# Optimization experiments

Measured on AMD Instinct MI355X. Metric: run time of the kernel, lower is better.

The kernel has to match this reference:

```python
import jax, jax.numpy as jnp
import numpy as np

B, IN, U = 16, 1024, 1024


def _wSw(W, S):
    # W: [i,u], S: [b,i,i] -> W^T S W : [b,u,u]
    return jnp.einsum('iu,bij,jv->buv', W, S, W)


def _xSx(x, Wsig):
    # (sum_i x_i^2) * W_Sigma, broadcast over batch
    return jnp.sum(x * x, axis=1)[:, None, None] * Wsig


def _trS(S, Wsig):
    return jnp.trace(S, axis1=1, axis2=2)[:, None, None] * Wsig


def _hadamard_sigma(s1, s2, m1, m2):
    # s1*s2 + diag(m1) s2 diag(m1) + diag(m2) s1 diag(m2)
    return (s1 * s2
            + m1[:, :, None] * s2 * m1[:, None, :]
            + m2[:, :, None] * s1 * m2[:, None, :])


def _act_sigma(g, S):
    # S * outer(g, g)
    return S * (g[:, :, None] * g[:, None, :])


def setup_inputs() -> dict:
    key = jax.random.key(0)
    ks = jax.random.split(key, 16)
    f32 = jnp.float32
    init_mu, ini_sigma = 0.05, -4.6
    inp = {
        'mu_inputs': jax.random.normal(ks[0], (B, IN), f32),
        'sigma_inputs': 0.01 * jax.random.normal(ks[1], (B, IN, IN), f32),
        'prev_state': 0.1 * jax.random.normal(ks[2], (B, U), f32),
        'Sigma_state': 0.01 * jax.random.normal(ks[3], (B, U, U), f32),
        'U_z': init_mu * jax.random.normal(ks[4], (IN, U), f32),
        'uz_sigma': jnp.full((U,), ini_sigma, f32),
        'W_z': init_mu * jax.random.normal(ks[5], (U, U), f32),
        'wz_sigma': jnp.full((U,), ini_sigma, f32),
        'U_r': init_mu * jax.random.normal(ks[6], (IN, U), f32),
        'ur_sigma': jnp.full((U,), ini_sigma, f32),
        'W_r': init_mu * jax.random.normal(ks[7], (U, U), f32),
        'wr_sigma': jnp.full((U,), ini_sigma, f32),
        'U_h': init_mu * jax.random.normal(ks[8], (IN, U), f32),
        'uh_sigma': jnp.full((U,), ini_sigma, f32),
        'W_h': init_mu * jax.random.normal(ks[9], (U, U), f32),
        'wh_sigma': jnp.full((U,), ini_sigma, f32),
    }
    return inp


def reference(mu_inputs, sigma_inputs, prev_state, Sigma_state,
              U_z, uz_sigma, W_z, wz_sigma,
              U_r, ur_sigma, W_r, wr_sigma,
              U_h, uh_sigma, W_h, wh_sigma):
    sp = jax.nn.softplus
    # ---- z gate ----
    pre_z = mu_inputs @ U_z + prev_state @ W_z
    z = jax.nn.sigmoid(pre_z)
    Uz_S, Wz_S = jnp.diag(sp(uz_sigma)), jnp.diag(sp(wz_sigma))
    Sigma_zz = (_wSw(U_z, sigma_inputs) + _xSx(mu_inputs, Uz_S) + _trS(sigma_inputs, Uz_S)
                + _wSw(W_z, Sigma_state) + _xSx(prev_state, Wz_S) + _trS(Sigma_state, Wz_S))
    Sigma_z = _act_sigma(z * (1.0 - z), Sigma_zz)  # analytic d sigmoid
    # ---- r gate ----
    pre_r = mu_inputs @ U_r + prev_state @ W_r
    r = jax.nn.sigmoid(pre_r)
    Ur_S, Wr_S = jnp.diag(sp(ur_sigma)), jnp.diag(sp(wr_sigma))
    Sigma_rr = (_wSw(U_r, sigma_inputs) + _xSx(mu_inputs, Ur_S) + _trS(sigma_inputs, Ur_S)
                + _wSw(W_r, Sigma_state) + _xSx(prev_state, Wr_S) + _trS(Sigma_state, Wr_S))
    Sigma_r = _act_sigma(r * (1.0 - r), Sigma_rr)
    # ---- h gate ----
    sr = prev_state * r
    pre_h = mu_inputs @ U_h + sr @ W_h
    h = jnp.tanh(pre_h)
    Uh_S, Wh_S = jnp.diag(sp(uh_sigma)), jnp.diag(sp(wh_sigma))
    sigma_g = _hadamard_sigma(Sigma_state, Sigma_r, prev_state, r)
    Sigma_hh = (_wSw(U_h, sigma_inputs) + _xSx(mu_inputs, Uh_S) + _trS(sigma_inputs, Uh_S)
                + _wSw(W_h, sigma_g) + _xSx(sr, Wh_S) + _trS(sigma_g, Wh_S))
    Sigma_h = _act_sigma(1.0 - h * h, Sigma_hh)  # analytic d tanh
    # ---- combine ----
    mu_out = z * prev_state + (1.0 - z) * h
    sigma_a = _hadamard_sigma(Sigma_z, Sigma_state, z, prev_state)
    sigma_b = _hadamard_sigma(Sigma_z, Sigma_h, 1.0 - z, h)
    sigma_ab = Sigma_z * (prev_state[:, :, None] * h[:, None, :])
    sigma_abT = Sigma_z * (h[:, :, None] * prev_state[:, None, :])
    Sigma_out = sigma_a + sigma_b - sigma_ab - sigma_abT
    Sigma_out = jnp.where(jnp.isfinite(Sigma_out), Sigma_out, jnp.zeros_like(Sigma_out))
    eye = jnp.eye(Sigma_out.shape[-1], dtype=bool)
    Sigma_out = jnp.where(eye, jnp.abs(Sigma_out), Sigma_out)
    return mu_out, Sigma_out
```

## Files before the change

kernel.cpp:

```cpp
#include <hip/hip_runtime.h>
#include <math.h>


#define B_  16
#define N_  1024
#define NN_ (1024*1024)

typedef __bf16 bf16x8 __attribute__((ext_vector_type(8)));
typedef float  f32x4  __attribute__((ext_vector_type(4)));
typedef unsigned short ushort8v __attribute__((ext_vector_type(8)));

__device__ __forceinline__ unsigned short f2bf(float f) {
  union { float f; unsigned int u; } v; v.f = f;
  unsigned int r = v.u + 0x7fffu + ((v.u >> 16) & 1u);
  return (unsigned short)(r >> 16);
}
__device__ __forceinline__ float bf2f(unsigned short h) {
  union { unsigned int u; float f; } v; v.u = ((unsigned int)h) << 16;
  return v.f;
}
__device__ __forceinline__ float f4get(const float4& v, int q) {
  return q == 0 ? v.x : (q == 1 ? v.y : (q == 2 ? v.z : v.w));
}
__device__ __forceinline__ unsigned short u4get(const ushort4& v, int q) {
  return q == 0 ? v.x : (q == 1 ? v.y : (q == 2 ? v.z : v.w));
}

__device__ __forceinline__ void gload_lds16(const void* g, void* l) {
  __builtin_amdgcn_global_load_lds((__attribute__((address_space(1))) void*)g,
                                   (__attribute__((address_space(3))) void*)l,
                                   16, 0, 0);
}

#define MFMA_ __builtin_amdgcn_mfma_f32_16x16x32_bf16

template<int OMODE, int PAIR>
__global__ __launch_bounds__(512)
void gemm8p(const unsigned short* __restrict__ A, int lda, long aStride, int koffA,
            const unsigned short* __restrict__ Bm, const unsigned short* __restrict__ Bm2,
            int ldb, long bStride, int K,
            void* __restrict__ Out, int ldo, long oStride, int noff,
            const float* __restrict__ act,
            const float* __restrict__ spU, const float* __restrict__ spW,
            const float* __restrict__ dU, const float* __restrict__ dW)
{
  __shared__ __align__(16) char ldsb[131072];
  const int id = blockIdx.x;
  const int xcd = id & 7, rest = id >> 3;
  const int mt = rest & 3, pp = rest >> 2;
  const int panel = xcd + (pp << 3);
  const int nt = panel & 3;
  const int b  = (panel >> 2) & 15;
  const int ps = PAIR ? (panel >> 6) : 0;
  const unsigned short* Bsel = (PAIR && ps) ? Bm2 : Bm;
  const int kofx = koffA + (ps ? 1024 : 0);
  const int nofx = noff  + (ps ? 1024 : 0);
  const int mbase = mt << 8, nbase = nt << 8;
  const int tid = threadIdx.x, lane = tid & 63, w = tid >> 6;
  const int wm = w >> 2, wn = w & 3;
  const int NT = K >> 6;

  f32x4 acc[8][4];
  const f32x4 zero4 = {0.f, 0.f, 0.f, 0.f};
#pragma unroll
  for (int i = 0; i < 8; i++)
#pragma unroll
    for (int j = 0; j < 4; j++) acc[i][j] = zero4;

  const int l3 = lane >> 3, l7 = lane & 7;
  const int posg = l7 ^ l3;
  const int gr = (l3 << 1) + (posg >> 2);
  const int gc = (posg & 3) << 3;
  const int bi0 = w << 1, bi1 = bi0 + 1;
  const int rS0 = ((bi0 >> 1) << 4) + gr, cS0 = ((bi0 & 1) << 5) + gc;
  const int rS1 = ((bi1 >> 1) << 4) + gr, cS1 = ((bi1 & 1) << 5) + gc;
  const unsigned short* Ab = A + (size_t)b * aStride + (size_t)mbase * lda + kofx;
  const unsigned short* Bb = Bsel + (size_t)b * bStride + (size_t)nbase * ldb;
  const int d0 = w << 11, d1 = (w << 11) + 1024;

  auto SA = [&](int tt, int h) {
    char* dst = ldsb + ((tt & 1) << 16) + (h << 14);
    const unsigned short* s = Ab + (size_t)(h << 7) * lda + ((size_t)tt << 6);
    gload_lds16(s + (size_t)rS0 * lda + cS0, dst + d0);
    gload_lds16(s + (size_t)rS1 * lda + cS1, dst + d1);
  };
  auto SB = [&](int tt, int h) {
    char* dst = ldsb + ((tt & 1) << 16) + 32768 + (h << 14);
    const unsigned short* s = Bb + (size_t)(h << 7) * ldb + ((size_t)tt << 6);
    gload_lds16(s + (size_t)rS0 * ldb + cS0, dst + d0);
    gload_lds16(s + (size_t)rS1 * ldb + cS1, dst + d1);
  };

  const int lrow = lane & 15, c4 = lane >> 4;
  const int aoff = ((lrow >> 1) << 7) + (((((lrow & 1) << 2) | c4) ^ (lrow >> 1)) << 4);
  const int abase = wm << 14;
  const int bbase = 32768 + ((wn >> 1) << 14);
  const int brg   = (wn & 1) << 2;
  auto LDA = [&](const char* pb, int mi, int ks) -> bf16x8 {
    return *(const bf16x8*)(pb + abase + (((mi << 1) + ks) << 10) + aoff);
  };
  auto LDB = [&](const char* pb, int ni, int ks) -> bf16x8 {
    return *(const bf16x8*)(pb + bbase + ((((brg + ni) << 1) + ks) << 10) + aoff);
  };

  SA(0, 0); SA(0, 1); SB(0, 0); SB(0, 1);
  if (NT > 1) { SB(1, 0); SB(1, 1); }
  asm volatile("s_waitcnt vmcnt(4)" ::: "memory");
  __builtin_amdgcn_sched_barrier(0);
  __builtin_amdgcn_s_barrier();
  __builtin_amdgcn_sched_barrier(0);

  bf16x8 av[4], bv[4];
  for (int kt = 0; kt < NT; ++kt) {
    const char* pb = ldsb + ((kt & 1) << 16);
#pragma unroll
    for (int mi = 0; mi < 4; mi++) av[mi] = LDA(pb, mi, 0);
#pragma unroll
    for (int ni = 0; ni < 4; ni++) bv[ni] = LDB(pb, ni, 0);
    if (kt + 1 < NT) SA(kt + 1, 0);
    __builtin_amdgcn_s_barrier();
    asm volatile("s_waitcnt lgkmcnt(0)" ::: "memory");
    __builtin_amdgcn_sched_barrier(0);
    __builtin_amdgcn_s_setprio(1);
#pragma unroll
    for (int ni = 0; ni < 4; ni++)
#pragma unroll
      for (int mi = 0; mi < 4; mi++)
        acc[mi][ni] = MFMA_(av[mi], bv[ni], acc[mi][ni], 0, 0, 0);
    __builtin_amdgcn_s_setprio(0);
    __builtin_amdgcn_sched_barrier(0);
    __builtin_amdgcn_s_barrier();
#pragma unroll
    for (int mi = 0; mi < 4; mi++) av[mi] = LDA(pb, 4 + mi, 0);
    if (kt + 1 < NT) SA(kt + 1, 1);
    __builtin_amdgcn_s_barrier();
    asm volatile("s_waitcnt lgkmcnt(0)" ::: "memory");
    __builtin_amdgcn_sched_barrier(0);
    __builtin_amdgcn_s_setprio(1);
#pragma unroll
    for (int ni = 0; ni < 4; ni++)
#pragma unroll
      for (int mi = 0; mi < 4; mi++)
        acc[4 + mi][ni] = MFMA_(av[mi], bv[ni], acc[4 + mi][ni], 0, 0, 0);
    __builtin_amdgcn_s_setprio(0);
    __builtin_amdgcn_sched_barrier(0);
    __builtin_amdgcn_s_barrier();
#pragma unroll
    for (int mi = 0; mi < 4; mi++) av[mi] = LDA(pb, mi, 1);
#pragma unroll
    for (int ni = 0; ni < 4; ni++) bv[ni] = LDB(pb, ni, 1);
    __builtin_amdgcn_s_barrier();
    asm volatile("s_waitcnt lgkmcnt(0)" ::: "memory");
    __builtin_amdgcn_sched_barrier(0);
    __builtin_amdgcn_s_setprio(1);
#pragma unroll
    for (int ni = 0; ni < 4; ni++)
#pragma unroll
      for (int mi = 0; mi < 4; mi++)
        acc[mi][ni] = MFMA_(av[mi], bv[ni], acc[mi][ni], 0, 0, 0);
    __builtin_amdgcn_s_setprio(0);
    __builtin_amdgcn_sched_barrier(0);
    __builtin_amdgcn_s_barrier();
#pragma unroll
    for (int mi = 0; mi < 4; mi++) av[mi] = LDA(pb, 4 + mi, 1);
    if (kt + 2 < NT) {
      SB(kt + 2, 0); SB(kt + 2, 1);
      asm volatile("s_waitcnt vmcnt(4)" ::: "memory");
    } else {
      asm volatile("s_waitcnt vmcnt(0)" ::: "memory");
    }
    __builtin_amdgcn_s_barrier();
    asm volatile("s_waitcnt lgkmcnt(0)" ::: "memory");
    __builtin_amdgcn_sched_barrier(0);
    __builtin_amdgcn_s_setprio(1);
#pragma unroll
    for (int ni = 0; ni < 4; ni++)
#pragma unroll
      for (int mi = 0; mi < 4; mi++)
        acc[4 + mi][ni] = MFMA_(av[mi], bv[ni], acc[4 + mi][ni], 0, 0, 0);
    __builtin_amdgcn_s_setprio(0);
    __builtin_amdgcn_sched_barrier(0);
    __builtin_amdgcn_s_barrier();
  }

  if (OMODE == 2) {
    const float* actb = act + b * N_;
    const float dUb = dU[b], dWb = dW[b];
#pragma unroll
    for (int mi = 0; mi < 8; mi++) {
      const int u0 = mbase + wm * 128 + mi * 16 + ((lane >> 4) << 2);
#pragma unroll
      for (int ni = 0; ni < 4; ni++) {
        const int v = nbase + wn * 64 + ni * 16 + (lane & 15);
        const float avv = actb[v];
#pragma unroll
        for (int r = 0; r < 4; r++) {
          const int u = u0 + r;
          float val = acc[mi][ni][r];
          if (u == v) val += dUb * spU[u] + dWb * spW[u];
          val *= actb[u] * avv;
          ((float*)Out)[(size_t)b * oStride + (size_t)u * ldo + v] = val;
        }
      }
    }
  } else {
    __syncthreads();
    unsigned short* scr = (unsigned short*)(ldsb + w * 16384);
    const float* actb = (OMODE == 1) ? (act + b * N_) : nullptr;
    float dUb = 0.f, dWb = 0.f;
    if (OMODE == 1) { dUb = dU[b]; dWb = dW[b]; }
#pragma unroll
    for (int mi = 0; mi < 8; mi++) {
      const int rl0 = mi * 16 + ((lane >> 4) << 2);
#pragma unroll
      for (int ni = 0; ni < 4; ni++) {
        const int cl = ni * 16 + (lane & 15);
#pragma unroll
        for (int r = 0; r < 4; r++) {
          const int rl = rl0 + r;
          float val = acc[mi][ni][r];
          if (OMODE == 1) {
            const int u = mbase + wm * 128 + rl, v = nbase + wn * 64 + cl;
            if (u == v) val += dUb * spU[u] + dWb * spW[u];
            val *= actb[u] * actb[v];
          }
          scr[rl * 64 + ((((cl >> 3) ^ (rl & 7))) << 3) + (cl & 7)] = f2bf(val);
        }
      }
    }
    asm volatile("s_waitcnt lgkmcnt(0)" ::: "memory");
    __builtin_amdgcn_sched_barrier(0);
    unsigned short* ob = (unsigned short*)Out + (size_t)b * oStride
        + (size_t)(mbase + wm * 128) * ldo + nofx + nbase + wn * 64;
#pragma unroll
    for (int pq = 0; pq < 16; pq++) {
      const int row = pq * 8 + (lane >> 3);
      const int ch = (lane & 7) ^ (row & 7);
      ushort8v vv = *(const ushort8v*)&scr[row * 64 + ((lane & 7) << 3)];
      *(ushort8v*)(ob + (size_t)row * ldo + ch * 8) = vv;
    }
  }
}


__global__ void conv_bf16(const float* __restrict__ in, unsigned short* __restrict__ out, int n4)
{
  int i = blockIdx.x * 256 + threadIdx.x;
  const int stride = gridDim.x * 256;
  for (; i < n4; i += stride) {
    const float4 v = ((const float4*)in)[i];
    ushort4 o;
    o.x = f2bf(v.x); o.y = f2bf(v.y); o.z = f2bf(v.z); o.w = f2bf(v.w);
    ((ushort4*)out)[i] = o;
  }
}

__global__ void build_AT(const float* __restrict__ Uz, const float* __restrict__ Wz,
                         const float* __restrict__ Ur, const float* __restrict__ Wr,
                         const float* __restrict__ Uh, const float* __restrict__ Wh,
                         unsigned short* __restrict__ AT)
{
  __shared__ float tile[32][33];
  const int g = blockIdx.z;
  const float* U = g == 0 ? Uz : (g == 1 ? Ur : Uh);
  const float* W = g == 0 ? Wz : (g == 1 ? Wr : Wh);
  const int u0  = blockIdx.x * 32;
  const int k0g = blockIdx.y * 32;
  const float* src = (k0g >= 1024) ? W : U;
  const int kloc = k0g & 1023;
  const int tx = threadIdx.x & 31, ty = threadIdx.x >> 5;
  unsigned short* out = AT + (size_t)g * N_ * 2048;
#pragma unroll
  for (int i = 0; i < 32; i += 8) tile[ty + i][tx] = src[(size_t)(kloc + ty + i) * N_ + u0 + tx];
  __syncthreads();
#pragma unroll
  for (int i = 0; i < 32; i += 8)
    out[(size_t)(u0 + ty + i) * 2048 + k0g + tx] = f2bf(tile[tx][ty + i]);
}

__global__ void softplus6(const float* a0, const float* a1, const float* a2,
                          const float* a3, const float* a4, const float* a5,
                          float* __restrict__ sp)
{
  const float* src[6] = {a0, a1, a2, a3, a4, a5};
  const int g = blockIdx.x;
  const float* s = src[g];
  for (int i = threadIdx.x; i < N_; i += 256) {
    float x = s[i];
    sp[g * N_ + i] = (x > 20.f) ? x : log1pf(expf(x));
  }
}

__global__ void scalars1(const float* __restrict__ mu, const float* __restrict__ prev,
                         const float* __restrict__ sin_, const float* __restrict__ Sst,
                         float* __restrict__ dA, float* __restrict__ dBzr)
{
  __shared__ float red[256];
  const int b = blockIdx.x;
  float s1 = 0.f, s2 = 0.f;
  for (int i = threadIdx.x; i < N_; i += 256) {
    const float m = mu[b * N_ + i];
    s1 += m * m + sin_[(size_t)b * NN_ + (size_t)i * (N_ + 1)];
    const float p = prev[b * N_ + i];
    s2 += p * p + Sst[(size_t)b * NN_ + (size_t)i * (N_ + 1)];
  }
  red[threadIdx.x] = s1; __syncthreads();
  for (int s = 128; s > 0; s >>= 1) { if (threadIdx.x < s) red[threadIdx.x] += red[threadIdx.x + s]; __syncthreads(); }
  if (threadIdx.x == 0) dA[b] = red[0];
  __syncthreads();
  red[threadIdx.x] = s2; __syncthreads();
  for (int s = 128; s > 0; s >>= 1) { if (threadIdx.x < s) red[threadIdx.x] += red[threadIdx.x + s]; __syncthreads(); }
  if (threadIdx.x == 0) dBzr[b] = red[0];
}

__global__ __launch_bounds__(256)
void gate_pre2(const float* __restrict__ x1, const float* __restrict__ x2,
               const float* __restrict__ U0, const float* __restrict__ W0,
               const float* __restrict__ U1, const float* __restrict__ W1,
               float* __restrict__ Ppart)
{
  const int g  = blockIdx.z;
  const int ks = blockIdx.y;
  const int out = blockIdx.x * 256 + threadIdx.x;
  const int b = out >> 10, col = out & 1023;
  const float* x = (ks < 4) ? x1 : x2;
  const float* Wm = (g == 0) ? ((ks < 4) ? U0 : W0) : ((ks < 4) ? U1 : W1);
  const int k0 = (ks & 3) * 256;
  const float* xb = x + b * N_ + k0;
  const float* wp = Wm + (size_t)k0 * N_ + col;
  float acc = 0.f;
#pragma unroll 8
  for (int k = 0; k < 256; k++)
    acc += xb[k] * wp[(size_t)k * N_];
  Ppart[(g * 8 + ks) * (B_ * N_) + out] = acc;
}

__global__ void gate_act2(const float* __restrict__ P,
                          float* __restrict__ z, float* __restrict__ gz,
                          float* __restrict__ r, float* __restrict__ gr)
{
  const int out = blockIdx.x * 256 + threadIdx.x;
  float a0 = 0.f, a1 = 0.f;
#pragma unroll
  for (int ks = 0; ks < 8; ks++) {
    a0 += P[ks * (B_ * N_) + out];
    a1 += P[(8 + ks) * (B_ * N_) + out];
  }
  const float s0 = 1.f / (1.f + expf(-a0));
  const float s1 = 1.f / (1.f + expf(-a1));
  z[out] = s0; gz[out] = s0 * (1.f - s0);
  r[out] = s1; gr[out] = s1 * (1.f - s1);
}

__global__ __launch_bounds__(256)
void gate_pre1(const float* __restrict__ x1, const float* __restrict__ x2,
               const float* __restrict__ U0, const float* __restrict__ W0,
               float* __restrict__ Ppart)
{
  const int ks = blockIdx.y;
  const int out = blockIdx.x * 256 + threadIdx.x;
  const int b = out >> 10, col = out & 1023;
  const float* x = (ks < 4) ? x1 : x2;
  const float* Wm = (ks < 4) ? U0 : W0;
  const int k0 = (ks & 3) * 256;
  const float* xb = x + b * N_ + k0;
  const float* wp = Wm + (size_t)k0 * N_ + col;
  float acc = 0.f;
#pragma unroll 8
  for (int k = 0; k < 256; k++)
    acc += xb[k] * wp[(size_t)k * N_];
  Ppart[ks * (B_ * N_) + out] = acc;
}

__global__ void gate_act1(const float* __restrict__ P,
                          float* __restrict__ h, float* __restrict__ gh)
{
  const int out = blockIdx.x * 256 + threadIdx.x;
  float a0 = 0.f;
#pragma unroll
  for (int ks = 0; ks < 8; ks++) a0 += P[ks * (B_ * N_) + out];
  const float s = tanhf(a0);
  h[out] = s; gh[out] = 1.f - s * s;
}

__global__ void sr_csr(const float* __restrict__ prev, const float* __restrict__ r,
                       float* __restrict__ sr, float* __restrict__ csr)
{
  __shared__ float red[256];
  const int b = blockIdx.x;
  float s = 0.f;
  for (int i = threadIdx.x; i < N_; i += 256) {
    const float v = prev[b * N_ + i] * r[b * N_ + i];
    sr[b * N_ + i] = v;
    s += v * v;
  }
  red[threadIdx.x] = s; __syncthreads();
  for (int k = 128; k > 0; k >>= 1) { if (threadIdx.x < k) red[threadIdx.x] += red[threadIdx.x + k]; __syncthreads(); }
  if (threadIdx.x == 0) csr[b] = red[0];
}

__global__ void hadamard_sg(const float* __restrict__ Sst, unsigned short* __restrict__ Sg,
                            const float* __restrict__ prev, const float* __restrict__ r)
{
  const size_t idx = ((size_t)blockIdx.x * 256 + threadIdx.x) * 4;
  const int b = (int)(idx >> 20);
  const int rem = (int)(idx & (NN_ - 1));
  const int i = rem >> 10, j0 = rem & 1023;
  const float pi = prev[b * N_ + i], ri = r[b * N_ + i];
  const float4  ss  = *(const float4*)(Sst + (size_t)b * NN_ + rem);
  const ushort4 sr4 = *(const ushort4*)(Sg + (size_t)b * NN_ + rem);
  ushort4 o;
  unsigned short* op = (unsigned short*)&o;
#pragma unroll
  for (int q = 0; q < 4; q++) {
    const float srv = bf2f(u4get(sr4, q));
    const float stv = f4get(ss, q);
    const float pj = prev[b * N_ + j0 + q];
    const float rj = r[b * N_ + j0 + q];
    op[q] = f2bf(stv * srv + pi * pj * srv + ri * rj * stv);
  }
  *(ushort4*)(Sg + (size_t)b * NN_ + rem) = o;
}

__global__ void scalars2(const unsigned short* __restrict__ Sg,
                         const float* __restrict__ csr, float* __restrict__ dBh)
{
  __shared__ float red[256];
  const int b = blockIdx.x;
  float s = 0.f;
  for (int i = threadIdx.x; i < N_; i += 256)
    s += bf2f(Sg[(size_t)b * NN_ + (size_t)i * (N_ + 1)]);
  red[threadIdx.x] = s; __syncthreads();
  for (int k = 128; k > 0; k >>= 1) { if (threadIdx.x < k) red[threadIdx.x] += red[threadIdx.x + k]; __syncthreads(); }
  if (threadIdx.x == 0) dBh[b] = red[0] + csr[b];
}

__global__ void mu_kernel(const float* __restrict__ z, const float* __restrict__ prev,
                          const float* __restrict__ h, float* __restrict__ mu_out)
{
  const int i = blockIdx.x * 256 + threadIdx.x;
  const float zz = z[i];
  mu_out[i] = zz * prev[i] + (1.f - zz) * h[i];
}

__global__ void combine(const unsigned short* __restrict__ Sz, const float* __restrict__ Sst,
                        const float* __restrict__ z, const float* __restrict__ prev,
                        const float* __restrict__ h, float* __restrict__ SigOut)
{
  const int row = blockIdx.x;
  const int b = row >> 10, u = row & 1023;
  const float zu = z[b * N_ + u], pu = prev[b * N_ + u], hu = h[b * N_ + u];
  const size_t base = (size_t)b * NN_ + (size_t)u * N_;
  const int j0 = threadIdx.x * 4;
  const ushort4 s4 = *(const ushort4*)(Sz + base + j0);
  const float4 sh = *(const float4*)(SigOut + base + j0);
  const float4 st = *(const float4*)(Sst + base + j0);
  const float4 zv = *(const float4*)(z + b * N_ + j0);
  const float4 pv = *(const float4*)(prev + b * N_ + j0);
  const float4 hv = *(const float4*)(h + b * N_ + j0);
  float o[4];
#pragma unroll
  for (int q = 0; q < 4; q++) {
    const int v = j0 + q;
    const float sz  = bf2f(u4get(s4, q));
    const float shh = f4get(sh, q);
    const float stt = f4get(st, q);
    const float zvv = f4get(zv, q);
    const float pvv = f4get(pv, q);
    const float hvv = f4get(hv, q);
    float res = sz * stt + zu * zvv * stt + pu * pvv * sz
              + sz * shh + (1.f - zu) * (1.f - zvv) * shh + hu * hvv * sz
              - sz * (pu * hvv) - sz * (hu * pvv);
    if (!isfinite(res)) res = 0.f;
    if (u == v) res = fabsf(res);
    o[q] = res;
  }
  float4 ov; ov.x = o[0]; ov.y = o[1]; ov.z = o[2]; ov.w = o[3];
  *(float4*)(SigOut + base + j0) = ov;
}


extern "C" void kernel_launch(void* const* d_in, const int* in_sizes, int n_in,
                              void* d_out, int out_size, void* d_ws, size_t ws_size,
                              hipStream_t stream)
{
  const float* mu   = (const float*)d_in[0];
  const float* sin_ = (const float*)d_in[1];
  const float* prev = (const float*)d_in[2];
  const float* Sst  = (const float*)d_in[3];
  const float* Uz = (const float*)d_in[4];  const float* uzs = (const float*)d_in[5];
  const float* Wz = (const float*)d_in[6];  const float* wzs = (const float*)d_in[7];
  const float* Ur = (const float*)d_in[8];  const float* urs = (const float*)d_in[9];
  const float* Wr = (const float*)d_in[10]; const float* wrs = (const float*)d_in[11];
  const float* Uh = (const float*)d_in[12]; const float* uhs = (const float*)d_in[13];
  const float* Wh = (const float*)d_in[14]; const float* whs = (const float*)d_in[15];

  char* ws = (char*)d_ws;
  size_t off = 0;
  auto take = [&](size_t bytes) -> char* {
    char* p = ws + off;
    off = (off + bytes + 255) & ~(size_t)255;
    return p;
  };
  unsigned short* Tcm = (unsigned short*)take((size_t)B_ * 2048 * 1024 * 2);
  unsigned short* Sz  = (unsigned short*)take((size_t)B_ * NN_ * 2);
  unsigned short* Sg  = (unsigned short*)take((size_t)B_ * NN_ * 2);
  unsigned short* AT  = (unsigned short*)take((size_t)3 * N_ * 2048 * 2);
  float* Ppart = (float*)take((size_t)16 * B_ * N_ * 4);
  float* sp   = (float*)take(6 * N_ * 4);
  float* z    = (float*)take(B_ * N_ * 4);
  float* gz   = (float*)take(B_ * N_ * 4);
  float* rr   = (float*)take(B_ * N_ * 4);
  float* gr   = (float*)take(B_ * N_ * 4);
  float* h    = (float*)take(B_ * N_ * 4);
  float* gh   = (float*)take(B_ * N_ * 4);
  float* sr   = (float*)take(B_ * N_ * 4);
  float* dA   = (float*)take(64);
  float* dBzr = (float*)take(64);
  float* dBh  = (float*)take(64);
  float* csr  = (float*)take(64);
  if (off > ws_size) return;

  float* mu_out = (float*)d_out;
  float* SigOut = (float*)d_out + (size_t)B_ * N_;
  unsigned short* SinH = (unsigned short*)SigOut;
  unsigned short* SstH = (unsigned short*)SigOut + (size_t)B_ * NN_;

  const unsigned short* ATz = AT;
  const unsigned short* ATr = AT + (size_t)N_ * 2048;
  const unsigned short* ATh = AT + (size_t)2 * N_ * 2048;

  conv_bf16<<<2048, 256, 0, stream>>>(sin_, SinH, B_ * NN_ / 4);
  conv_bf16<<<2048, 256, 0, stream>>>(Sst,  SstH, B_ * NN_ / 4);
  softplus6<<<6, 256, 0, stream>>>(uzs, wzs, urs, wrs, uhs, whs, sp);
  scalars1<<<16, 256, 0, stream>>>(mu, prev, sin_, Sst, dA, dBzr);
  build_AT<<<dim3(32, 64, 3), 256, 0, stream>>>(Uz, Wz, Ur, Wr, Uh, Wh, AT);
  gate_pre2<<<dim3(64, 8, 2), 256, 0, stream>>>(mu, prev, Uz, Wz, Ur, Wr, Ppart);
  gate_act2<<<64, 256, 0, stream>>>(Ppart, z, gz, rr, gr);
  sr_csr<<<16, 256, 0, stream>>>(prev, rr, sr, csr);
  gate_pre1<<<dim3(64, 8), 256, 0, stream>>>(mu, sr, Uh, Wh, Ppart);
  gate_act1<<<64, 256, 0, stream>>>(Ppart, h, gh);

  const long tS = (long)2048 * 1024;

  gemm8p<0, 1><<<512, 512, 0, stream>>>(ATz, 2048, 0, 0, SinH, SstH, 1024, (long)NN_, 1024,
                                        Tcm, 2048, tS, 0, nullptr, nullptr, nullptr, nullptr, nullptr);
  gemm8p<1, 0><<<256, 512, 0, stream>>>(ATz, 2048, 0, 0, Tcm, nullptr, 2048, tS, 2048,
                                        Sz, 1024, (long)NN_, 0, gz, sp + 0, sp + 1024, dA, dBzr);
  gemm8p<0, 1><<<512, 512, 0, stream>>>(ATr, 2048, 0, 0, SinH, SstH, 1024, (long)NN_, 1024,
                                        Tcm, 2048, tS, 0, nullptr, nullptr, nullptr, nullptr, nullptr);
  gemm8p<1, 0><<<256, 512, 0, stream>>>(ATr, 2048, 0, 0, Tcm, nullptr, 2048, tS, 2048,
                                        Sg, 1024, (long)NN_, 0, gr, sp + 2048, sp + 3072, dA, dBzr);
  hadamard_sg<<<16384, 256, 0, stream>>>(Sst, Sg, prev, rr);
  scalars2<<<16, 256, 0, stream>>>(Sg, csr, dBh);
  gemm8p<0, 1><<<512, 512, 0, stream>>>(ATh, 2048, 0, 0, SinH, Sg, 1024, (long)NN_, 1024,
                                        Tcm, 2048, tS, 0, nullptr, nullptr, nullptr, nullptr, nullptr);
  gemm8p<2, 0><<<256, 512, 0, stream>>>(ATh, 2048, 0, 0, Tcm, nullptr, 2048, tS, 2048,
                                        SigOut, 1024, (long)NN_, 0, gh, sp + 4096, sp + 5120, dA, dBh);
  mu_kernel<<<64, 256, 0, stream>>>(z, prev, h, mu_out);
  combine<<<16384, 256, 0, stream>>>(Sz, Sst, z, prev, h, SigOut);
}
```

Before: 575.1 us.

## Double-buffer MFMA operand registers to overlap LDS reads with matrix math

Splits the A/B fragment registers into two sets so each LDS read phase fetches operands for the next MFMA cluster while the current cluster computes. It drops the explicit lgkmcnt(0) waits before each MFMA block and prefetches the next k-tile's first fragments at the end of the iteration. The aim is to hide LDS latency behind MFMA work. The cost is more VGPRs, and correctness relies on the compiler inserting the needed waits.

```diff
diff --git a/kernel.cpp b/kernel.cpp
--- a/kernel.cpp
+++ b/kernel.cpp
@@ -33,6 +33,9 @@
 }
 
 #define MFMA_ __builtin_amdgcn_mfma_f32_16x16x32_bf16
+#define SBAR_()  do { __builtin_amdgcn_sched_barrier(0); \
+                      __builtin_amdgcn_s_barrier(); \
+                      __builtin_amdgcn_sched_barrier(0); } while (0)
 
 template<int OMODE, int PAIR>
 __global__ __launch_bounds__(512)
@@ -106,81 +109,77 @@
   SA(0, 0); SA(0, 1); SB(0, 0); SB(0, 1);
   if (NT > 1) { SB(1, 0); SB(1, 1); }
   asm volatile("s_waitcnt vmcnt(4)" ::: "memory");
+  SBAR_();
+
+  bf16x8 avA[4], avB[4], bvA[4], bvB[4];
+#pragma unroll
+  for (int i = 0; i < 4; i++) avB[i] = LDA(ldsb, i, 0);
+#pragma unroll
+  for (int i = 0; i < 4; i++) bvB[i] = LDB(ldsb, i, 0);
   __builtin_amdgcn_sched_barrier(0);
-  __builtin_amdgcn_s_barrier();
-  __builtin_amdgcn_sched_barrier(0);
-
-  bf16x8 av[4], bv[4];
+
   for (int kt = 0; kt < NT; ++kt) {
     const char* pb = ldsb + ((kt & 1) << 16);
-#pragma unroll
-    for (int mi = 0; mi < 4; mi++) av[mi] = LDA(pb, mi, 0);
-#pragma unroll
-    for (int ni = 0; ni < 4; ni++) bv[ni] = LDB(pb, ni, 0);
+    const char* pn = ldsb + (((kt + 1) & 1) << 16);
+#pragma unroll
+    for (int i = 0; i < 4; i++) avA[i] = LDA(pb, 4 + i, 0);
     if (kt + 1 < NT) SA(kt + 1, 0);
-    __builtin_amdgcn_s_barrier();
-    asm volatile("s_waitcnt lgkmcnt(0)" ::: "memory");
-    __builtin_amdgcn_sched_barrier(0);
+    SBAR_();
     __builtin_amdgcn_s_setprio(1);
 #pragma unroll
     for (int ni = 0; ni < 4; ni++)
 #pragma unroll
       for (int mi = 0; mi < 4; mi++)
-        acc[mi][ni] = MFMA_(av[mi], bv[ni], acc[mi][ni], 0, 0, 0);
+        acc[mi][ni] = MFMA_(avB[mi], bvB[ni], acc[mi][ni], 0, 0, 0);
     __builtin_amdgcn_s_setprio(0);
-    __builtin_amdgcn_sched_barrier(0);
-    __builtin_amdgcn_s_barrier();
-#pragma unroll
-    for (int mi = 0; mi < 4; mi++) av[mi] = LDA(pb, 4 + mi, 0);
+    SBAR_();
+#pragma unroll
+    for (int i = 0; i < 4; i++) avB[i] = LDA(pb, i, 1);
+#pragma unroll
+    for (int i = 0; i < 4; i++) bvA[i] = LDB(pb, i, 1);
     if (kt + 1 < NT) SA(kt + 1, 1);
-    __builtin_amdgcn_s_barrier();
-    asm volatile("s_waitcnt lgkmcnt(0)" ::: "memory");
-    __builtin_amdgcn_sched_barrier(0);
+    SBAR_();
     __builtin_amdgcn_s_setprio(1);
 #pragma unroll
     for (int ni = 0; ni < 4; ni++)
 #pragma unroll
       for (int mi = 0; mi < 4; mi++)
-        acc[4 + mi][ni] = MFMA_(av[mi], bv[ni], acc[4 + mi][ni], 0, 0, 0);
+        acc[4 + mi][ni] = MFMA_(avA[mi], bvB[ni], acc[4 + mi][ni], 0, 0, 0);
     __builtin_amdgcn_s_setprio(0);
-    __builtin_amdgcn_sched_barrier(0);
-    __builtin_amdgcn_s_barrier();
-#pragma unroll
-    for (int mi = 0; mi < 4; mi++) av[mi] = LDA(pb, mi, 1);
-#pragma unroll
-    for (int ni = 0; ni < 4; ni++) bv[ni] = LDB(pb, ni, 1);
-    __builtin_amdgcn_s_barrier();
-    asm volatile("s_waitcnt lgkmcnt(0)" ::: "memory");
-    __builtin_amdgcn_sched_barrier(0);
+    SBAR_();
+#pragma unroll
+    for (int i = 0; i < 4; i++) avA[i] = LDA(pb, 4 + i, 1);
+    SBAR_();
     __builtin_amdgcn_s_setprio(1);
 #pragma unroll
     for (int ni = 0; ni < 4; ni++)
 #pragma unroll
       for (int mi = 0; mi < 4; mi++)
-        acc[mi][ni] = MFMA_(av[mi], bv[ni], acc[mi][ni], 0, 0, 0);
+        acc[mi][ni] = MFMA_(avB[mi], bvA[ni], acc[mi][ni], 0, 0, 0);
     __builtin_amdgcn_s_setprio(0);
-    __builtin_amdgcn_sched_barrier(0);
-    __builtin_amdgcn_s_barrier();
-#pragma unroll
-    for (int mi = 0; mi < 4; mi++) av[mi] = LDA(pb, 4 + mi, 1);
+    SBAR_();
     if (kt + 2 < NT) {
       SB(kt + 2, 0); SB(kt + 2, 1);
       asm volatile("s_waitcnt vmcnt(4)" ::: "memory");
-    } else {
+    } else if (kt + 1 < NT) {
       asm volatile("s_waitcnt vmcnt(0)" ::: "memory");
     }
-    __builtin_amdgcn_s_barrier();
-    asm volatile("s_waitcnt lgkmcnt(0)" ::: "memory");
+    SBAR_();
+    if (kt + 1 < NT) {
+#pragma unroll
+      for (int i = 0; i < 4; i++) avB[i] = LDA(pn, i, 0);
+#pragma unroll
+      for (int i = 0; i < 4; i++) bvB[i] = LDB(pn, i, 0);
+    }
     __builtin_amdgcn_sched_barrier(0);
     __builtin_amdgcn_s_setprio(1);
 #pragma unroll
     for (int ni = 0; ni < 4; ni++)
 #pragma unroll
       for (int mi = 0; mi < 4; mi++)
-        acc[4 + mi][ni] = MFMA_(av[mi], bv[ni], acc[4 + mi][ni], 0, 0, 0);
+        acc[4 + mi][ni] = MFMA_(avA[mi], bvA[ni], acc[4 + mi][ni], 0, 0, 0);
     __builtin_amdgcn_s_setprio(0);
-    __builtin_amdgcn_sched_barrier(0);
-    __builtin_amdgcn_s_barrier();
+    SBAR_();
   }
 
   if (OMODE == 2) {
```

Result: no change. 574.7 us (-0.1%).
